# Optimization experiments

Measured on AMD Instinct MI355X. Metric: run time of the kernel, lower is better.

The kernel has to match this reference:

```python
import jax, jax.numpy as jnp
import numpy as np

N0 = 100000
N1 = 100000
K = 16
D_MODEL = 64
D_ATTN = 32
H = 4


def setup_inputs() -> dict:
    key = jax.random.key(0)
    ks = jax.random.split(key, 12)
    inp = {
        "coords0": jax.random.normal(ks[0], (N0, 3), jnp.float32),
        "coords1": jax.random.normal(ks[1], (N1, 3), jnp.float32),
        "feats0": jax.random.normal(ks[2], (N0, D_MODEL), jnp.float32),
        "feats1": jax.random.normal(ks[3], (N1, D_MODEL), jnp.float32),
        "knn_idxs": jax.random.randint(ks[4], (1, N1, K), 0, N0, jnp.int64 if jax.config.jax_enable_x64 else jnp.int32),
        # Linear params (PyTorch Linear: y = x @ W.T + b; stored here already transposed as [in, out])
        "Wq": jax.random.normal(ks[5], (D_MODEL, D_ATTN), jnp.float32) / np.sqrt(D_MODEL),
        "bq": jnp.zeros((D_ATTN,), jnp.float32),
        "Wk": jax.random.normal(ks[6], (D_MODEL + 3, D_ATTN), jnp.float32) / np.sqrt(D_MODEL + 3),
        "bk": jnp.zeros((D_ATTN,), jnp.float32),
        "Wv": jax.random.normal(ks[7], (D_MODEL + 3, D_MODEL), jnp.float32) / np.sqrt(D_MODEL + 3),
        "bv": jnp.zeros((D_MODEL,), jnp.float32),
    }
    return inp


def reference(coords0, coords1, feats0, feats1, knn_idxs, Wq, bq, Wk, bk, Wv, bv):
    idx = knn_idxs[0]  # [N1, K] neighbor indices into cloud 0
    n1, k_ = idx.shape
    dh_attn = D_ATTN // H   # per-head query/key depth
    dh_val = D_MODEL // H   # per-head value depth

    # Irregular gathers from source cloud
    g_feats = feats0[idx]                         # [N1, K, D_MODEL]
    rel = coords0[idx] - coords1[:, None, :]      # [N1, K, 3] relative coords
    kv_in = jnp.concatenate([g_feats, rel], axis=-1)  # [N1, K, D_MODEL+3]

    # Projections + head split
    q = (feats1 @ Wq + bq).reshape(n1, H, dh_attn)                    # [N1, H, dh]
    k = (kv_in @ Wk + bk).reshape(n1, k_, H, dh_attn).transpose(0, 2, 1, 3)  # [N1, H, K, dh]
    v = (kv_in @ Wv + bv).reshape(n1, k_, H, dh_val).transpose(0, 2, 1, 3)   # [N1, H, K, dv]

    # Attention over K neighbors per point
    attn = jnp.einsum('nhd,nhkd->nhk', q, k) / np.sqrt(dh_attn).astype(np.float32)
    attn = jax.nn.softmax(attn, axis=-1)          # [N1, H, K]
    out = jnp.einsum('nhk,nhkd->nhd', attn, v)    # [N1, H, dv]
    out = out.reshape(n1, -1)                     # [N1, D_MODEL]
    return out, knn_idxs
```

## Files before the change

### kernel.cpp

```cpp
#include <hip/hip_runtime.h>


using half8   = __attribute__((ext_vector_type(8))) _Float16;
using floatx4 = __attribute__((ext_vector_type(4))) float;

template<int CTRL>
__device__ __forceinline__ float dppAdd(float x) {
    int y = __builtin_amdgcn_update_dpp(0, __float_as_int(x), CTRL, 0xF, 0xF, true);
    return x + __int_as_float(y);
}
__device__ __forceinline__ float rowSum16(float x) {
    x = dppAdd<0x121>(x);
    x = dppAdd<0x122>(x);
    x = dppAdd<0x124>(x);
    x = dppAdd<0x128>(x);
    return x;
}

__global__ __launch_bounds__(256) void prep_weights(
    const float* __restrict__ Wq, const float* __restrict__ Wk,
    const float* __restrict__ Wv,
    _Float16* __restrict__ fragKV, _Float16* __restrict__ fragQ)
{
    const int base = blockIdx.x * 256 + threadIdx.x;
    for (int e = base; e < 6144; e += 2048) {
        int j = e & 7, ln = (e >> 3) & 63, h = (e >> 9) & 1, t = e >> 10;
        int k = h * 32 + ((ln >> 4) * 8) + j;
        int n = t * 16 + (ln & 15);
        float v = (n < 32) ? Wk[k * 32 + n] : Wv[k * 64 + (n - 32)];
        fragKV[e] = (_Float16)v;
    }
    for (int e = base; e < 2048; e += 2048) {
        int j = e & 7, ln = (e >> 3) & 63, h = (e >> 9) & 1, t = e >> 10;
        int k = h * 32 + ((ln >> 4) * 8) + j;
        int n = t * 16 + (ln & 15);
        fragQ[e] = (_Float16)Wq[k * 32 + n];
    }
}

__global__ __launch_bounds__(256, 4) void proj_fused(
    const float* __restrict__ feats0, const float* __restrict__ feats1,
    const _Float16* __restrict__ fragKV, const _Float16* __restrict__ fragQ,
    const float* __restrict__ bq, const float* __restrict__ bk,
    const float* __restrict__ bv,
    _Float16* __restrict__ KVh, float* __restrict__ Qf,
    int n0, int n1, int nbKV, int nbQ, int tiles0, int tiles1)
{
    __shared__ __align__(16) _Float16 sFrag[6144];
    __shared__ __align__(16) _Float16 sOut[6144];

    const int tid  = threadIdx.x;
    const int wave = tid >> 6;
    const int lane = tid & 63;
    const int l15  = lane & 15;
    const int quad = lane >> 4;
    const int bid  = (int)blockIdx.x;

    if (bid < nbKV) {
        half8* sF8 = (half8*)sFrag;
        const half8* fk8 = (const half8*)fragKV;
        for (int c = tid; c < 768; c += 256) sF8[c] = fk8[c];
        __syncthreads();
        const half8* bf = (const half8*)sFrag;

        float bb[6];
        #pragma unroll
        for (int t = 0; t < 6; t++) {
            int n = t * 16 + l15;
            bb[t] = (n < 32) ? bk[n] : bv[n - 32];
        }

        for (int tile = bid; tile < tiles0; tile += nbKV) {
            const int rowBase = tile * 64;
            const int m0   = rowBase + wave * 16;
            const int row  = m0 + l15;
            const int rowc = (row < n0) ? row : (n0 - 1);
            const floatx4* X4 = (const floatx4*)(feats0 + (size_t)rowc * 64);
            floatx4 f0 = X4[quad * 2 + 0], f1 = X4[quad * 2 + 1];
            floatx4 f2 = X4[quad * 2 + 8], f3 = X4[quad * 2 + 9];
            half8 a0, a1;
            a0[0]=(_Float16)f0.x; a0[1]=(_Float16)f0.y; a0[2]=(_Float16)f0.z; a0[3]=(_Float16)f0.w;
            a0[4]=(_Float16)f1.x; a0[5]=(_Float16)f1.y; a0[6]=(_Float16)f1.z; a0[7]=(_Float16)f1.w;
            a1[0]=(_Float16)f2.x; a1[1]=(_Float16)f2.y; a1[2]=(_Float16)f2.z; a1[3]=(_Float16)f2.w;
            a1[4]=(_Float16)f3.x; a1[5]=(_Float16)f3.y; a1[6]=(_Float16)f3.z; a1[7]=(_Float16)f3.w;

            floatx4 acc[6];
            #pragma unroll
            for (int t = 0; t < 6; t++) acc[t] = (floatx4){bb[t], bb[t], bb[t], bb[t]};
            #pragma unroll
            for (int t = 0; t < 6; t++) {
                acc[t] = __builtin_amdgcn_mfma_f32_16x16x32_f16(a0, bf[(t*2+0)*64 + lane], acc[t], 0,0,0);
                acc[t] = __builtin_amdgcn_mfma_f32_16x16x32_f16(a1, bf[(t*2+1)*64 + lane], acc[t], 0,0,0);
            }

            #pragma unroll
            for (int t = 0; t < 6; t++)
                #pragma unroll
                for (int r = 0; r < 4; r++)
                    sOut[(wave * 16 + quad * 4 + r) * 96 + t * 16 + l15] = (_Float16)acc[t][r];

            const half8* so8 = (const half8*)sOut + wave * 192;
            half8* dst = (half8*)(KVh + (size_t)rowBase * 96) + wave * 192;
            #pragma unroll
            for (int u = 0; u < 3; u++) {
                int c = lane + u * 64;
                int r = c / 12;
                if (m0 + r < n0) dst[c] = so8[c];
            }
        }
    } else {
        half8* sF8 = (half8*)sFrag;
        const half8* fq8 = (const half8*)fragQ;
        for (int c = tid; c < 256; c += 256) sF8[c] = fq8[c];
        __syncthreads();
        const half8* bf = (const half8*)sFrag;

        float bb[2];
        #pragma unroll
        for (int t = 0; t < 2; t++) bb[t] = bq[t * 16 + l15];

        for (int tile = bid - nbKV; tile < tiles1; tile += nbQ) {
            const int rowBase = tile * 64;
            const int m0   = rowBase + wave * 16;
            const int row  = m0 + l15;
            const int rowc = (row < n1) ? row : (n1 - 1);
            const floatx4* X4 = (const floatx4*)(feats1 + (size_t)rowc * 64);
            floatx4 f0 = X4[quad * 2 + 0], f1 = X4[quad * 2 + 1];
            floatx4 f2 = X4[quad * 2 + 8], f3 = X4[quad * 2 + 9];
            half8 a0, a1;
            a0[0]=(_Float16)f0.x; a0[1]=(_Float16)f0.y; a0[2]=(_Float16)f0.z; a0[3]=(_Float16)f0.w;
            a0[4]=(_Float16)f1.x; a0[5]=(_Float16)f1.y; a0[6]=(_Float16)f1.z; a0[7]=(_Float16)f1.w;
            a1[0]=(_Float16)f2.x; a1[1]=(_Float16)f2.y; a1[2]=(_Float16)f2.z; a1[3]=(_Float16)f2.w;
            a1[4]=(_Float16)f3.x; a1[5]=(_Float16)f3.y; a1[6]=(_Float16)f3.z; a1[7]=(_Float16)f3.w;

            floatx4 acc[2];
            #pragma unroll
            for (int t = 0; t < 2; t++) acc[t] = (floatx4){bb[t], bb[t], bb[t], bb[t]};
            #pragma unroll
            for (int t = 0; t < 2; t++) {
                acc[t] = __builtin_amdgcn_mfma_f32_16x16x32_f16(a0, bf[(t*2+0)*64 + lane], acc[t], 0,0,0);
                acc[t] = __builtin_amdgcn_mfma_f32_16x16x32_f16(a1, bf[(t*2+1)*64 + lane], acc[t], 0,0,0);
            }
            #pragma unroll
            for (int t = 0; t < 2; t++)
                #pragma unroll
                for (int r = 0; r < 4; r++) {
                    int ro = m0 + quad * 4 + r;
                    if (ro < n1) Qf[(size_t)ro * 32 + t * 16 + l15] = acc[t][r];
                }
        }
    }
}

__global__ __launch_bounds__(256, 4) void attn_kernel(
    const float* __restrict__ coords0, const float* __restrict__ coords1,
    const int*   __restrict__ knn,
    const float* __restrict__ Qf, const _Float16* __restrict__ KVh,
    const float* __restrict__ Wk, const float* __restrict__ Wv,
    float* __restrict__ out, float* __restrict__ outIdx, int n1)
{
    __shared__ __align__(16) float sQ[16][36];
    __shared__ float sWk3[3][32];
    __shared__ float sWv3[3][64];
    __shared__ __align__(16) float sT[16][12];
    __shared__ __align__(16) int   sIdx[16][16];
    __shared__ __align__(16) float sA[16][68];

    const int tid = threadIdx.x;
    for (int e = tid; e < 288; e += 256) {
        if (e < 96) ((float*)sWk3)[e] = Wk[2048 + e];
        else        ((float*)sWv3)[e - 96] = Wv[4096 + (e - 96)];
    }
    if (tid < 128) {
        int pt = tid >> 3, c4 = tid & 7;
        int r = blockIdx.x * 16 + pt;
        if (r >= n1) r = n1 - 1;
        ((floatx4*)&sQ[pt][0])[c4] = ((const floatx4*)Qf)[(size_t)r * 8 + c4];
    }
    __syncthreads();

    const int p = tid >> 4;
    const int j = tid & 15;
    const int n = blockIdx.x * 16 + p;
    const bool valid = (n < n1);
    const int nc = valid ? n : (n1 - 1);

    const int idx = knn[nc * 16 + j];

    const half8* kr = (const half8*)(KVh + (size_t)idx * 96);
    half8 k8_0 = kr[0], k8_1 = kr[1], k8_2 = kr[2], k8_3 = kr[3];

    const float r0 = coords0[idx * 3 + 0] - coords1[nc * 3 + 0];
    const float r1 = coords0[idx * 3 + 1] - coords1[nc * 3 + 1];
    const float r2 = coords0[idx * 3 + 2] - coords1[nc * 3 + 2];

    const int g    = j & 7;
    const int hf   = j >> 3;
    const int h    = g >> 1;
    const int slot = ((j & 1) << 3) + (j >> 1);

    sIdx[p][slot] = idx;

    if (j < 12) {
        int c = j >> 2, h2 = j & 3;
        float t = 0.f;
        #pragma unroll
        for (int i = 0; i < 8; i++)
            t = fmaf(sWk3[c][h2 * 8 + i], sQ[p][h2 * 8 + i], t);
        sT[p][j] = t;
    }

    const int4* si4 = (const int4*)&sIdx[p][hf * 8];
    int4 viA = si4[0], viB = si4[1];
    int vIdx[8] = {viA.x, viA.y, viA.z, viA.w, viB.x, viB.y, viB.z, viB.w};
    half8 v8[8];
    #pragma unroll
    for (int s = 0; s < 8; s++)
        v8[s] = *(const half8*)(KVh + (size_t)vIdx[s] * 96 + 32 + g * 8);

    const floatx4* t4 = (const floatx4*)&sT[p][0];
    floatx4 tc0 = t4[0], tc1 = t4[1], tc2 = t4[2];

    const float scale = 0.35355339059327373f;
    float a_h[4];
    {
        half8 k8[4] = {k8_0, k8_1, k8_2, k8_3};
        #pragma unroll
        for (int h2 = 0; h2 < 4; h2++) {
            floatx4 q0 = ((const floatx4*)&sQ[p][0])[h2 * 2 + 0];
            floatx4 q1 = ((const floatx4*)&sQ[p][0])[h2 * 2 + 1];
            float acc = r0 * tc0[h2] + r1 * tc1[h2] + r2 * tc2[h2];
            acc = fmaf(q0[0], (float)k8[h2][0], acc);
            acc = fmaf(q0[1], (float)k8[h2][1], acc);
            acc = fmaf(q0[2], (float)k8[h2][2], acc);
            acc = fmaf(q0[3], (float)k8[h2][3], acc);
            acc = fmaf(q1[0], (float)k8[h2][4], acc);
            acc = fmaf(q1[1], (float)k8[h2][5], acc);
            acc = fmaf(q1[2], (float)k8[h2][6], acc);
            acc = fmaf(q1[3], (float)k8[h2][7], acc);
            float e = __expf(acc * scale);
            float ssum = rowSum16(e);
            a_h[h2] = e * __builtin_amdgcn_rcpf(ssum);
        }
    }

    sA[p][0 * 16 + slot] = a_h[0];
    sA[p][1 * 16 + slot] = a_h[1];
    sA[p][2 * 16 + slot] = a_h[2];
    sA[p][3 * 16 + slot] = a_h[3];

    if (valid) outIdx[n * 16 + j] = (float)idx;

    float rbs0, rbs1, rbs2;
    {
        float s00 = rowSum16(a_h[0] * r0), s01 = rowSum16(a_h[1] * r0);
        float s02 = rowSum16(a_h[2] * r0), s03 = rowSum16(a_h[3] * r0);
        rbs0 = (h == 0) ? s00 : (h == 1) ? s01 : (h == 2) ? s02 : s03;
        float s10 = rowSum16(a_h[0] * r1), s11 = rowSum16(a_h[1] * r1);
        float s12 = rowSum16(a_h[2] * r1), s13 = rowSum16(a_h[3] * r1);
        rbs1 = (h == 0) ? s10 : (h == 1) ? s11 : (h == 2) ? s12 : s13;
        float s20 = rowSum16(a_h[0] * r2), s21 = rowSum16(a_h[1] * r2);
        float s22 = rowSum16(a_h[2] * r2), s23 = rowSum16(a_h[3] * r2);
        rbs2 = (h == 0) ? s20 : (h == 1) ? s21 : (h == 2) ? s22 : s23;
    }

    const floatx4* a4 = (const floatx4*)&sA[p][h * 16 + hf * 8];
    floatx4 aw0 = a4[0], aw1 = a4[1];
    float av[8] = {aw0[0], aw0[1], aw0[2], aw0[3], aw1[0], aw1[1], aw1[2], aw1[3]};

    float acc8[8] = {0,0,0,0,0,0,0,0};
    #pragma unroll
    for (int s = 0; s < 8; s++)
        #pragma unroll
        for (int i = 0; i < 8; i++)
            acc8[i] = fmaf(av[s], (float)v8[s][i], acc8[i]);

    #pragma unroll
    for (int i = 0; i < 8; i++) acc8[i] = dppAdd<0x128>(acc8[i]);

    #pragma unroll
    for (int i = 0; i < 8; i++)
        acc8[i] += rbs0 * sWv3[0][8 * g + i] + rbs1 * sWv3[1][8 * g + i] + rbs2 * sWv3[2][8 * g + i];

    if (valid) {
        floatx4 st = { acc8[hf * 4 + 0], acc8[hf * 4 + 1], acc8[hf * 4 + 2], acc8[hf * 4 + 3] };
        ((floatx4*)out)[(size_t)n * 16 + g * 2 + hf] = st;
    }
}

extern "C" void kernel_launch(void* const* d_in, const int* in_sizes, int n_in,
                              void* d_out, int out_size, void* d_ws, size_t ws_size,
                              hipStream_t stream) {
    const float* coords0 = (const float*)d_in[0];
    const float* coords1 = (const float*)d_in[1];
    const float* feats0  = (const float*)d_in[2];
    const float* feats1  = (const float*)d_in[3];
    const int*   knn     = (const int*)d_in[4];
    const float* Wq      = (const float*)d_in[5];
    const float* bq      = (const float*)d_in[6];
    const float* Wk      = (const float*)d_in[7];
    const float* bk      = (const float*)d_in[8];
    const float* Wv      = (const float*)d_in[9];
    const float* bv      = (const float*)d_in[10];

    const int n0 = in_sizes[0] / 3;
    const int n1 = in_sizes[1] / 3;

    char* ws = (char*)d_ws;
    _Float16* KVh = (_Float16*)ws;
    float*    Qf  = (float*)(ws + (size_t)n0 * 96 * 2);
    _Float16* fragKV = (_Float16*)(ws + (size_t)n0 * 96 * 2 + (size_t)n1 * 32 * 4);
    _Float16* fragQ  = fragKV + 6144;

    float* out    = (float*)d_out;
    float* outIdx = out + (size_t)n1 * 64;

    const int tiles0 = (n0 + 63) / 64;
    const int tiles1 = (n1 + 63) / 64;
    const int nbKV = 512, nbQ = 256;

    prep_weights<<<8, 256, 0, stream>>>(Wq, Wk, Wv, fragKV, fragQ);
    proj_fused<<<nbKV + nbQ, 256, 0, stream>>>(feats0, feats1, fragKV, fragQ,
                                               bq, bk, bv, KVh, Qf,
                                               n0, n1, nbKV, nbQ, tiles0, tiles1);
    attn_kernel<<<(n1 + 15) / 16, 256, 0, stream>>>(coords0, coords1, knn,
                                                    Qf, KVh, Wk, Wv, out, outIdx, n1);
}
```

Before: 189.3 us.

## Redistribute QK score work per head and pad gathered coords to float4

The attention kernel now assigns each lane one head-chunk of K for four neighbors, instead of one neighbor with all four heads. This replaces four 16-lane softmax reductions with one 4-lane reduction and collapses the twelve rowSum16 calls for the relative-coordinate weighted sum into three small group sums exchanged through shared memory. Separately, the prep kernel writes coords0 as padded float4 so each neighbor's coordinates come from one vector gather instead of three scalar loads. The cost is an extra pass over coords0, more workspace, extra shared-memory arrays, and a less coalesced K gather pattern.

After: 193.1 us. 1.02x slower.

```diff
diff --git a/kernel.cpp b/kernel.cpp
--- a/kernel.cpp
+++ b/kernel.cpp
@@ -16,25 +16,37 @@
     x = dppAdd<0x128>(x);
     return x;
 }
+__device__ __forceinline__ float grpSum4(float x) {
+    x = dppAdd<0x124>(x);
+    x = dppAdd<0x128>(x);
+    return x;
+}
 
 __global__ __launch_bounds__(256) void prep_weights(
     const float* __restrict__ Wq, const float* __restrict__ Wk,
-    const float* __restrict__ Wv,
-    _Float16* __restrict__ fragKV, _Float16* __restrict__ fragQ)
+    const float* __restrict__ Wv, const float* __restrict__ coords0,
+    _Float16* __restrict__ fragKV, _Float16* __restrict__ fragQ,
+    floatx4* __restrict__ cpad4, int n0)
 {
+    const int stride = gridDim.x * 256;
     const int base = blockIdx.x * 256 + threadIdx.x;
-    for (int e = base; e < 6144; e += 2048) {
+    for (int e = base; e < 6144; e += stride) {
         int j = e & 7, ln = (e >> 3) & 63, h = (e >> 9) & 1, t = e >> 10;
         int k = h * 32 + ((ln >> 4) * 8) + j;
         int n = t * 16 + (ln & 15);
         float v = (n < 32) ? Wk[k * 32 + n] : Wv[k * 64 + (n - 32)];
         fragKV[e] = (_Float16)v;
     }
-    for (int e = base; e < 2048; e += 2048) {
+    for (int e = base; e < 2048; e += stride) {
         int j = e & 7, ln = (e >> 3) & 63, h = (e >> 9) & 1, t = e >> 10;
         int k = h * 32 + ((ln >> 4) * 8) + j;
         int n = t * 16 + (ln & 15);
         fragQ[e] = (_Float16)Wq[k * 32 + n];
+    }
+    for (int i = base; i < n0; i += stride) {
+        floatx4 c = { coords0[(size_t)i*3+0], coords0[(size_t)i*3+1],
+                      coords0[(size_t)i*3+2], 0.f };
+        cpad4[i] = c;
     }
 }
 
@@ -153,7 +165,7 @@
 }
 
 __global__ __launch_bounds__(256, 4) void attn_kernel(
-    const float* __restrict__ coords0, const float* __restrict__ coords1,
+    const floatx4* __restrict__ cpad4, const float* __restrict__ coords1,
     const int*   __restrict__ knn,
     const float* __restrict__ Qf, const _Float16* __restrict__ KVh,
     const float* __restrict__ Wk, const float* __restrict__ Wv,
@@ -164,6 +176,9 @@
     __shared__ float sWv3[3][64];
     __shared__ __align__(16) float sT[16][12];
     __shared__ __align__(16) int   sIdx[16][16];
+    __shared__ __align__(16) int   sIdxLin[16][16];
+    __shared__ __align__(16) floatx4 sRel[16][16];
+    __shared__ __align__(16) floatx4 sRbar[16][4];
     __shared__ __align__(16) float sA[16][68];
 
     const int tid = threadIdx.x;
@@ -187,19 +202,21 @@
 
     const int idx = knn[nc * 16 + j];
 
-    const half8* kr = (const half8*)(KVh + (size_t)idx * 96);
-    half8 k8_0 = kr[0], k8_1 = kr[1], k8_2 = kr[2], k8_3 = kr[3];
-
-    const float r0 = coords0[idx * 3 + 0] - coords1[nc * 3 + 0];
-    const float r1 = coords0[idx * 3 + 1] - coords1[nc * 3 + 1];
-    const float r2 = coords0[idx * 3 + 2] - coords1[nc * 3 + 2];
-
     const int g    = j & 7;
     const int hf   = j >> 3;
-    const int h    = g >> 1;
+    const int h    = (j >> 1) & 3;
     const int slot = ((j & 1) << 3) + (j >> 1);
-
-    sIdx[p][slot] = idx;
+    const int sub  = j >> 2;
+    const int c4   = j & 3;
+
+    sIdxLin[p][j]  = idx;
+    sIdx[p][slot]  = idx;
+
+    floatx4 cg = cpad4[idx];
+    const float r0 = cg[0] - coords1[nc * 3 + 0];
+    const float r1 = cg[1] - coords1[nc * 3 + 1];
+    const float r2 = cg[2] - coords1[nc * 3 + 2];
+    sRel[p][j] = (floatx4){r0, r1, r2, 0.f};
 
     if (j < 12) {
         int c = j >> 2, h2 = j & 3;
@@ -209,6 +226,14 @@
             t = fmaf(sWk3[c][h2 * 8 + i], sQ[p][h2 * 8 + i], t);
         sT[p][j] = t;
     }
+
+    int nbIdx[4];
+    #pragma unroll
+    for (int t = 0; t < 4; t++) nbIdx[t] = sIdxLin[p][t * 4 + sub];
+    half8 kk[4];
+    #pragma unroll
+    for (int t = 0; t < 4; t++)
+        kk[t] = *(const half8*)(KVh + (size_t)nbIdx[t] * 96 + c4 * 8);
 
     const int4* si4 = (const int4*)&sIdx[p][hf * 8];
     int4 viA = si4[0], viB = si4[1];
@@ -218,56 +243,65 @@
     for (int s = 0; s < 8; s++)
         v8[s] = *(const half8*)(KVh + (size_t)vIdx[s] * 96 + 32 + g * 8);
 
-    const floatx4* t4 = (const floatx4*)&sT[p][0];
-    floatx4 tc0 = t4[0], tc1 = t4[1], tc2 = t4[2];
-
     const float scale = 0.35355339059327373f;
-    float a_h[4];
+    floatx4 qa = ((const floatx4*)&sQ[p][0])[c4 * 2 + 0];
+    floatx4 qb = ((const floatx4*)&sQ[p][0])[c4 * 2 + 1];
+    const float t0 = sT[p][0 * 4 + c4];
+    const float t1 = sT[p][1 * 4 + c4];
+    const float t2 = sT[p][2 * 4 + c4];
+
+    floatx4 rl[4];
+    float e[4];
+    #pragma unroll
+    for (int t = 0; t < 4; t++) {
+        rl[t] = sRel[p][t * 4 + sub];
+        float acc = rl[t][0] * t0 + rl[t][1] * t1 + rl[t][2] * t2;
+        acc = fmaf(qa[0], (float)kk[t][0], acc);
+        acc = fmaf(qa[1], (float)kk[t][1], acc);
+        acc = fmaf(qa[2], (float)kk[t][2], acc);
+        acc = fmaf(qa[3], (float)kk[t][3], acc);
+        acc = fmaf(qb[0], (float)kk[t][4], acc);
+        acc = fmaf(qb[1], (float)kk[t][5], acc);
+        acc = fmaf(qb[2], (float)kk[t][6], acc);
+        acc = fmaf(qb[3], (float)kk[t][7], acc);
+        e[t] = __expf(acc * scale);
+    }
+    float ssum = (e[0] + e[1]) + (e[2] + e[3]);
+    ssum = grpSum4(ssum);
+    const float rinv = __builtin_amdgcn_rcpf(ssum);
+
+    float a_t[4];
+    #pragma unroll
+    for (int t = 0; t < 4; t++) a_t[t] = e[t] * rinv;
+
+    #pragma unroll
+    for (int t = 0; t < 4; t++) {
+        int nb = t * 4 + sub;
+        sA[p][c4 * 16 + ((nb & 1) << 3) + (nb >> 1)] = a_t[t];
+    }
+
     {
-        half8 k8[4] = {k8_0, k8_1, k8_2, k8_3};
-        #pragma unroll
-        for (int h2 = 0; h2 < 4; h2++) {
-            floatx4 q0 = ((const floatx4*)&sQ[p][0])[h2 * 2 + 0];
-            floatx4 q1 = ((const floatx4*)&sQ[p][0])[h2 * 2 + 1];
-            float acc = r0 * tc0[h2] + r1 * tc1[h2] + r2 * tc2[h2];
-            acc = fmaf(q0[0], (float)k8[h2][0], acc);
-            acc = fmaf(q0[1], (float)k8[h2][1], acc);
-            acc = fmaf(q0[2], (float)k8[h2][2], acc);
-            acc = fmaf(q0[3], (float)k8[h2][3], acc);
-            acc = fmaf(q1[0], (float)k8[h2][4], acc);
-            acc = fmaf(q1[1], (float)k8[h2][5], acc);
-            acc = fmaf(q1[2], (float)k8[h2][6], acc);
-            acc = fmaf(q1[3], (float)k8[h2][7], acc);
-            float e = __expf(acc * scale);
-            float ssum = rowSum16(e);
-            a_h[h2] = e * __builtin_amdgcn_rcpf(ssum);
+        float pr0 = 0.f, pr1 = 0.f, pr2 = 0.f;
+        #pragma unroll
+        for (int t = 0; t < 4; t++) {
+            pr0 = fmaf(a_t[t], rl[t][0], pr0);
+            pr1 = fmaf(a_t[t], rl[t][1], pr1);
+            pr2 = fmaf(a_t[t], rl[t][2], pr2);
         }
-    }
-
-    sA[p][0 * 16 + slot] = a_h[0];
-    sA[p][1 * 16 + slot] = a_h[1];
-    sA[p][2 * 16 + slot] = a_h[2];
-    sA[p][3 * 16 + slot] = a_h[3];
+        pr0 = grpSum4(pr0);
+        pr1 = grpSum4(pr1);
+        pr2 = grpSum4(pr2);
+        if (sub == 0) sRbar[p][c4] = (floatx4){pr0, pr1, pr2, 0.f};
+    }
 
     if (valid) outIdx[n * 16 + j] = (float)idx;
-
-    float rbs0, rbs1, rbs2;
-    {
-        float s00 = rowSum16(a_h[0] * r0), s01 = rowSum16(a_h[1] * r0);
-        float s02 = rowSum16(a_h[2] * r0), s03 = rowSum16(a_h[3] * r0);
-        rbs0 = (h == 0) ? s00 : (h == 1) ? s01 : (h == 2) ? s02 : s03;
-        float s10 = rowSum16(a_h[0] * r1), s11 = rowSum16(a_h[1] * r1);
-        float s12 = rowSum16(a_h[2] * r1), s13 = rowSum16(a_h[3] * r1);
-        rbs1 = (h == 0) ? s10 : (h == 1) ? s11 : (h == 2) ? s12 : s13;
-        float s20 = rowSum16(a_h[0] * r2), s21 = rowSum16(a_h[1] * r2);
-        float s22 = rowSum16(a_h[2] * r2), s23 = rowSum16(a_h[3] * r2);
-        rbs2 = (h == 0) ? s20 : (h == 1) ? s21 : (h == 2) ? s22 : s23;
-    }
 
     const floatx4* a4 = (const floatx4*)&sA[p][h * 16 + hf * 8];
     floatx4 aw0 = a4[0], aw1 = a4[1];
     float av[8] = {aw0[0], aw0[1], aw0[2], aw0[3], aw1[0], aw1[1], aw1[2], aw1[3]};
 
+    floatx4 rb = sRbar[p][h];
+
     float acc8[8] = {0,0,0,0,0,0,0,0};
     #pragma unroll
     for (int s = 0; s < 8; s++)
@@ -280,7 +314,7 @@
 
     #pragma unroll
     for (int i = 0; i < 8; i++)
-        acc8[i] += rbs0 * sWv3[0][8 * g + i] + rbs1 * sWv3[1][8 * g + i] + rbs2 * sWv3[2][8 * g + i];
+        acc8[i] += rb[0] * sWv3[0][8 * g + i] + rb[1] * sWv3[1][8 * g + i] + rb[2] * sWv3[2][8 * g + i];
 
     if (valid) {
         floatx4 st = { acc8[hf * 4 + 0], acc8[hf * 4 + 1], acc8[hf * 4 + 2], acc8[hf * 4 + 3] };
@@ -309,7 +343,8 @@
     char* ws = (char*)d_ws;
     _Float16* KVh = (_Float16*)ws;
     float*    Qf  = (float*)(ws + (size_t)n0 * 96 * 2);
-    _Float16* fragKV = (_Float16*)(ws + (size_t)n0 * 96 * 2 + (size_t)n1 * 32 * 4);
+    floatx4*  cpad4 = (floatx4*)(ws + (size_t)n0 * 96 * 2 + (size_t)n1 * 32 * 4);
+    _Float16* fragKV = (_Float16*)(cpad4 + n0);
     _Float16* fragQ  = fragKV + 6144;
 
     float* out    = (float*)d_out;
@@ -319,10 +354,11 @@
     const int tiles1 = (n1 + 63) / 64;
     const int nbKV = 512, nbQ = 256;
 
-    prep_weights<<<8, 256, 0, stream>>>(Wq, Wk, Wv, fragKV, fragQ);
+    prep_weights<<<128, 256, 0, stream>>>(Wq, Wk, Wv, coords0,
+                                          fragKV, fragQ, cpad4, n0);
     proj_fused<<<nbKV + nbQ, 256, 0, stream>>>(feats0, feats1, fragKV, fragQ,
                                                bq, bk, bv, KVh, Qf,
                                                n0, n1, nbKV, nbQ, tiles0, tiles1);
-    attn_kernel<<<(n1 + 15) / 16, 256, 0, stream>>>(coords0, coords1, knn,
+    attn_kernel<<<(n1 + 15) / 16, 256, 0, stream>>>(cpad4, coords1, knn,
                                                     Qf, KVh, Wk, Wv, out, outIdx, n1);
 }
```
